# Kernel tuning notes

Hardware: AMD Instinct MI355X
Metric: run time of the kernel (lower is better)

Reference implementation:

```python
import jax, jax.numpy as jnp
import numpy as np


def setup_inputs() -> dict:
    key = jax.random.key(0)
    k1, k2 = jax.random.split(key)
    x = jax.random.normal(k1, (8, 128, 128, 128), dtype=jnp.float32)        # [N, C, H, W]
    codebook = jax.random.normal(k2, (256, 128), dtype=jnp.float32)         # [K, C] class_emb_vecs
    return {"x": x, "codebook": codebook}


def reference(x, codebook):
    # Brute-force 1-NN with p=2 (Euclidean), matching sklearn NearestNeighbors(brute, p=2).
    # argmin ||q - c||_2 == argmin (||q||^2 - 2 q.c + ||c||^2), so use the GEMM form.
    N, C, H, W = x.shape
    q = jnp.transpose(x, (0, 2, 3, 1)).reshape(-1, C)       # [N*H*W, C], matches x.reshape(-1, C) channel-last? 
    # NOTE: torch x.reshape(-1, C) on [N,C,H,W] flattens with C as the fastest-varying of the
    # leading dims only when memory layout is NCHW -> rows are (n, c_blocks)... Torch's
    # reshape(-1, C) actually slices contiguous groups of C elements along W. To be faithful
    # to x.reshape(-1, C) on a contiguous NCHW tensor:
    q = x.reshape(-1, C)                                     # [N*C*H*W/C, C] — same elements, same order as torch
    q_sq = jnp.sum(q * q, axis=1, keepdims=True)             # [M, 1]
    c_sq = jnp.sum(codebook * codebook, axis=1)              # [K]
    # squared distances: [M, K]
    d2 = q_sq - 2.0 * (q @ codebook.T) + c_sq[None, :]
    idx = jnp.argmin(d2, axis=1).astype(jnp.int32)           # [M]
    return idx.reshape(N, H, W)
```

## Files before the change

### kernel.cpp

```cpp
#include <hip/hip_runtime.h>
#include <hip/hip_bf16.h>


typedef __bf16 bf16x8 __attribute__((ext_vector_type(8)));
typedef float  floatx4 __attribute__((ext_vector_type(4)));

#define MFMA16 __builtin_amdgcn_mfma_f32_16x16x32_bf16

#define CSQ_OFF 1024
#define CBB_OFF 4096
#define T_FLAG  0.004f

__device__ __forceinline__ unsigned fmap(float f) {
    unsigned u = __float_as_uint(f);
    return (u & 0x80000000u) ? ~u : (u | 0x80000000u);
}
__device__ __forceinline__ float unfmap(unsigned u) {
    unsigned b = (u & 0x80000000u) ? (u ^ 0x80000000u) : ~u;
    return __uint_as_float(b);
}

__global__ void knn_prep(const float* __restrict__ cb, __bf16* __restrict__ cbB,
                         float* __restrict__ csq) {
    const int tid = threadIdx.x;
    const int id = blockIdx.x * 256 + tid;
    const int part = id >> 12;
    const int rem = id & 4095;
    const int t4 = rem >> 8;
    const int kb = (rem >> 6) & 3;
    const int ln = id & 63;
    const int n = t4 * 16 + (ln & 15);
    const int k0 = kb * 32 + (ln >> 4) * 8;
    const float* src = cb + (size_t)n * 128 + k0;
    union { __bf16 h[8]; uint4 u; } p;
#pragma unroll
    for (int j = 0; j < 8; ++j) {
        float f = src[j];
        __bf16 hh = (__bf16)f;
        p.h[j] = (part == 0) ? hh : (__bf16)(f - (float)hh);
    }
    *(uint4*)(cbB + (size_t)id * 8) = p.u;

    if (blockIdx.x == 0) {
        const float4* row = (const float4*)(cb + (size_t)tid * 128);
        float a0 = 0.f, a1 = 0.f, a2 = 0.f, a3 = 0.f;
#pragma unroll 8
        for (int j = 0; j < 32; ++j) {
            float4 v = row[j];
            a0 = fmaf(v.x, v.x, a0);
            a1 = fmaf(v.y, v.y, a1);
            a2 = fmaf(v.z, v.z, a2);
            a3 = fmaf(v.w, v.w, a3);
        }
        csq[tid] = (a0 + a1) + (a2 + a3);
    }
}

__global__ __launch_bounds__(256, 2) void knn_mfma(const float* __restrict__ x,
                                                   const float* __restrict__ cb,
                                                   const __bf16* __restrict__ cbB,
                                                   const float* __restrict__ csq_g,
                                                   int* __restrict__ out) {
    __shared__ __bf16 sB[32768];
    __shared__ float s_csq[256];
    __shared__ unsigned long long sWb[128];
    __shared__ unsigned long long sWs[128];
    __shared__ unsigned long long s_red[4];
    __shared__ int s_nf;
    __shared__ int s_flagq[64];

    const int tid = threadIdx.x;
    const int wave = tid >> 6;
    const int lane = tid & 63;
    const int mg = wave >> 1;
    const int ng = wave & 1;
    const int rl = lane & 15;
    const int kg = lane >> 4;

    s_csq[tid] = csq_g[tid];
    if (tid == 0) s_nf = 0;

    const float* xq = x + ((size_t)blockIdx.x * 64 + mg * 32) * 128;
    bf16x8 ah[2][4], al[2][4];
#pragma unroll
    for (int m = 0; m < 2; ++m) {
#pragma unroll
        for (int kb = 0; kb < 4; ++kb) {
            const float* s = xq + (size_t)(m * 16 + rl) * 128 + kb * 32 + kg * 8;
            float4 f0 = *(const float4*)(s);
            float4 f1 = *(const float4*)(s + 4);
            float f[8] = {f0.x, f0.y, f0.z, f0.w, f1.x, f1.y, f1.z, f1.w};
            union { __bf16 h[8]; bf16x8 v; } ph, pl;
#pragma unroll
            for (int j = 0; j < 8; ++j) {
                __bf16 hh = (__bf16)f[j];
                ph.h[j] = hh;
                pl.h[j] = (__bf16)(f[j] - (float)hh);
            }
            ah[m][kb] = ph.v;
            al[m][kb] = pl.v;
        }
    }

    {
        const uint4* src = (const uint4*)cbB;
        uint4* dst = (uint4*)sB;
#pragma unroll 4
        for (int i = 0; i < 16; ++i) dst[i * 256 + tid] = src[i * 256 + tid];
    }
    __syncthreads();

    floatx4 acc[2][8];
#pragma unroll
    for (int m = 0; m < 2; ++m)
#pragma unroll
        for (int t = 0; t < 8; ++t) acc[m][t] = (floatx4){0.f, 0.f, 0.f, 0.f};

#pragma unroll
    for (int kb = 0; kb < 4; ++kb) {
#pragma unroll
        for (int t = 0; t < 8; ++t) {
            const int t4 = ng * 8 + t;
            bf16x8 b = *(const bf16x8*)(sB + (((t4 * 4 + kb) * 64 + lane) * 8));
            acc[0][t] = MFMA16(ah[0][kb], b, acc[0][t], 0, 0, 0);
            acc[1][t] = MFMA16(ah[1][kb], b, acc[1][t], 0, 0, 0);
            acc[0][t] = MFMA16(al[0][kb], b, acc[0][t], 0, 0, 0);
            acc[1][t] = MFMA16(al[1][kb], b, acc[1][t], 0, 0, 0);
        }
    }
    __syncthreads();

    {
        const uint4* src = (const uint4*)(cbB + 32768);
        uint4* dst = (uint4*)sB;
#pragma unroll 4
        for (int i = 0; i < 16; ++i) dst[i * 256 + tid] = src[i * 256 + tid];
    }
    __syncthreads();

#pragma unroll
    for (int kb = 0; kb < 4; ++kb) {
#pragma unroll
        for (int t = 0; t < 8; ++t) {
            const int t4 = ng * 8 + t;
            bf16x8 b = *(const bf16x8*)(sB + (((t4 * 4 + kb) * 64 + lane) * 8));
            acc[0][t] = MFMA16(ah[0][kb], b, acc[0][t], 0, 0, 0);
            acc[1][t] = MFMA16(ah[1][kb], b, acc[1][t], 0, 0, 0);
        }
    }

    float cs[8];
#pragma unroll
    for (int t = 0; t < 8; ++t) cs[t] = s_csq[(ng * 8 + t) * 16 + rl];

#pragma unroll
    for (int m = 0; m < 2; ++m) {
#pragma unroll
        for (int r = 0; r < 4; ++r) {
            unsigned long long b = ~0ULL, s = ~0ULL;
#pragma unroll
            for (int t = 0; t < 8; ++t) {
                const int n = (ng * 8 + t) * 16 + rl;
                float score = fmaf(-2.0f, acc[m][t][r], cs[t]);
                unsigned long long key =
                    ((unsigned long long)fmap(score) << 32) | (unsigned)n;
                if (key < b) { s = b; b = key; }
                else if (key < s) { s = key; }
            }
#pragma unroll
            for (int d = 1; d < 16; d <<= 1) {
                unsigned long long ob = __shfl_xor(b, d);
                unsigned long long os = __shfl_xor(s, d);
                unsigned long long nb = ob < b ? ob : b;
                unsigned long long mx = ob < b ? b : ob;
                unsigned long long mn = os < s ? os : s;
                b = nb;
                s = mx < mn ? mx : mn;
            }
            if (rl == 0) {
                const int ql = mg * 32 + m * 16 + kg * 4 + r;
                sWb[ql * 2 + ng] = b;
                sWs[ql * 2 + ng] = s;
            }
        }
    }
    __syncthreads();

    if (tid < 64) {
        unsigned long long b0 = sWb[tid * 2 + 0], b1 = sWb[tid * 2 + 1];
        unsigned long long s0 = sWs[tid * 2 + 0], s1 = sWs[tid * 2 + 1];
        unsigned long long best = b0 < b1 ? b0 : b1;
        unsigned long long mx = b0 < b1 ? b1 : b0;
        unsigned long long mn = s0 < s1 ? s0 : s1;
        unsigned long long sec = mx < mn ? mx : mn;
        const size_t qg = (size_t)blockIdx.x * 64 + tid;
        out[qg] = (int)(unsigned)(best & 0xFFFFFFFFull);
        float f1 = unfmap((unsigned)(best >> 32));
        float f2 = unfmap((unsigned)(sec >> 32));
        if (f2 - f1 < T_FLAG) {
            int i = atomicAdd(&s_nf, 1);
            s_flagq[i] = tid;
        }
    }
    __syncthreads();

    const int nf = s_nf;
    for (int i = 0; i < nf; ++i) {
        const int lq = s_flagq[i];
        const size_t q = (size_t)blockIdx.x * 64 + lq;
        const float4* qr = (const float4*)(x + q * 128);
        const float4* cr = (const float4*)(cb + (size_t)tid * 128);
        float a0 = 0.f, a1 = 0.f, a2 = 0.f, a3 = 0.f;
#pragma unroll 8
        for (int c4 = 0; c4 < 32; ++c4) {
            float4 qv = qr[c4];
            float4 cv = cr[c4];
            a0 = fmaf(qv.x, cv.x, a0);
            a1 = fmaf(qv.y, cv.y, a1);
            a2 = fmaf(qv.z, cv.z, a2);
            a3 = fmaf(qv.w, cv.w, a3);
        }
        float dot = (a0 + a1) + (a2 + a3);
        float score = fmaf(-2.0f, dot, s_csq[tid]);
        unsigned long long key =
            ((unsigned long long)fmap(score) << 32) | (unsigned)tid;
#pragma unroll
        for (int d = 1; d < 64; d <<= 1) {
            unsigned long long o = __shfl_xor(key, d);
            key = o < key ? o : key;
        }
        if (lane == 0) s_red[wave] = key;
        __syncthreads();
        if (tid == 0) {
            unsigned long long b = s_red[0];
            unsigned long long o;
            o = s_red[1]; b = o < b ? o : b;
            o = s_red[2]; b = o < b ? o : b;
            o = s_red[3]; b = o < b ? o : b;
            out[q] = (int)(unsigned)(b & 0xFFFFFFFFull);
        }
        __syncthreads();
    }
}

extern "C" void kernel_launch(void* const* d_in, const int* in_sizes, int n_in,
                              void* d_out, int out_size, void* d_ws, size_t ws_size,
                              hipStream_t stream) {
    const float* x = (const float*)d_in[0];
    const float* cb = (const float*)d_in[1];
    int* out = (int*)d_out;

    char* ws = (char*)d_ws;
    float* csq = (float*)(ws + CSQ_OFF);
    __bf16* cbB = (__bf16*)(ws + CBB_OFF);

    const int M = in_sizes[0] / 128;

    knn_prep<<<32, 256, 0, stream>>>(cb, cbB, csq);
    knn_mfma<<<M / 64, 256, 0, stream>>>(x, cb, cbB, csq, out);
}
```

Measured before the change: 149.6 us.

## Split codebook into column chunks, give each wave its own rows, use direct-to-LDS loads

Each block now handles 128 queries instead of 64, and every wave owns 32 query rows across all 256 codes. The codebook is streamed through LDS in two chunks of 128 columns, each loaded with global_load_lds instead of register-staged copies. Top-2 results are merged across chunks per wave, which removes the cross-wave reduction, and the smaller LDS footprint allows three blocks per CU. The cost is twice as many LDS loads and barriers per block, half as many blocks, and higher register pressure under the tighter launch bound.

```diff
diff --git a/kernel.cpp b/kernel.cpp
--- a/kernel.cpp
+++ b/kernel.cpp
@@ -10,6 +10,13 @@
 #define CSQ_OFF 1024
 #define CBB_OFF 4096
 #define T_FLAG  0.004f
+
+typedef const __attribute__((address_space(1))) unsigned int* as1_u32p;
+typedef __attribute__((address_space(3))) unsigned int* as3_u32p;
+
+__device__ __forceinline__ void cp16_g2l(const void* g, void* l) {
+    __builtin_amdgcn_global_load_lds((as1_u32p)g, (as3_u32p)l, 16, 0, 0);
+}
 
 __device__ __forceinline__ unsigned fmap(float f) {
     unsigned u = __float_as_uint(f);
@@ -56,31 +63,28 @@
     }
 }
 
-__global__ __launch_bounds__(256, 2) void knn_mfma(const float* __restrict__ x,
+__global__ __launch_bounds__(256, 3) void knn_mfma(const float* __restrict__ x,
                                                    const float* __restrict__ cb,
                                                    const __bf16* __restrict__ cbB,
                                                    const float* __restrict__ csq_g,
                                                    int* __restrict__ out) {
-    __shared__ __bf16 sB[32768];
+    __shared__ __bf16 sB[16384];
     __shared__ float s_csq[256];
-    __shared__ unsigned long long sWb[128];
-    __shared__ unsigned long long sWs[128];
+    __shared__ unsigned long long sT2[4][32][2];
     __shared__ unsigned long long s_red[4];
     __shared__ int s_nf;
-    __shared__ int s_flagq[64];
+    __shared__ int s_flagq[128];
 
     const int tid = threadIdx.x;
     const int wave = tid >> 6;
     const int lane = tid & 63;
-    const int mg = wave >> 1;
-    const int ng = wave & 1;
     const int rl = lane & 15;
     const int kg = lane >> 4;
 
     s_csq[tid] = csq_g[tid];
     if (tid == 0) s_nf = 0;
 
-    const float* xq = x + ((size_t)blockIdx.x * 64 + mg * 32) * 128;
+    const float* xq = x + ((size_t)blockIdx.x * 128 + wave * 32) * 128;
     bf16x8 ah[2][4], al[2][4];
 #pragma unroll
     for (int m = 0; m < 2; ++m) {
@@ -101,13 +105,6 @@
             al[m][kb] = pl.v;
         }
     }
-
-    {
-        const uint4* src = (const uint4*)cbB;
-        uint4* dst = (uint4*)sB;
-#pragma unroll 4
-        for (int i = 0; i < 16; ++i) dst[i * 256 + tid] = src[i * 256 + tid];
-    }
     __syncthreads();
 
     floatx4 acc[2][8];
@@ -116,98 +113,117 @@
 #pragma unroll
         for (int t = 0; t < 8; ++t) acc[m][t] = (floatx4){0.f, 0.f, 0.f, 0.f};
 
-#pragma unroll
-    for (int kb = 0; kb < 4; ++kb) {
-#pragma unroll
-        for (int t = 0; t < 8; ++t) {
-            const int t4 = ng * 8 + t;
-            bf16x8 b = *(const bf16x8*)(sB + (((t4 * 4 + kb) * 64 + lane) * 8));
-            acc[0][t] = MFMA16(ah[0][kb], b, acc[0][t], 0, 0, 0);
-            acc[1][t] = MFMA16(ah[1][kb], b, acc[1][t], 0, 0, 0);
-            acc[0][t] = MFMA16(al[0][kb], b, acc[0][t], 0, 0, 0);
-            acc[1][t] = MFMA16(al[1][kb], b, acc[1][t], 0, 0, 0);
-        }
-    }
-    __syncthreads();
-
-    {
-        const uint4* src = (const uint4*)(cbB + 32768);
-        uint4* dst = (uint4*)sB;
-#pragma unroll 4
-        for (int i = 0; i < 16; ++i) dst[i * 256 + tid] = src[i * 256 + tid];
-    }
-    __syncthreads();
-
-#pragma unroll
-    for (int kb = 0; kb < 4; ++kb) {
-#pragma unroll
-        for (int t = 0; t < 8; ++t) {
-            const int t4 = ng * 8 + t;
-            bf16x8 b = *(const bf16x8*)(sB + (((t4 * 4 + kb) * 64 + lane) * 8));
-            acc[0][t] = MFMA16(ah[0][kb], b, acc[0][t], 0, 0, 0);
-            acc[1][t] = MFMA16(ah[1][kb], b, acc[1][t], 0, 0, 0);
-        }
-    }
-
-    float cs[8];
-#pragma unroll
-    for (int t = 0; t < 8; ++t) cs[t] = s_csq[(ng * 8 + t) * 16 + rl];
-
-#pragma unroll
-    for (int m = 0; m < 2; ++m) {
-#pragma unroll
-        for (int r = 0; r < 4; ++r) {
-            unsigned long long b = ~0ULL, s = ~0ULL;
+#pragma unroll 1
+    for (int nc = 0; nc < 2; ++nc) {
+        {
+            const __bf16* src = cbB + nc * 16384 + (size_t)tid * 8;
+            __bf16* dst = sB + tid * 8;
+#pragma unroll
+            for (int i = 0; i < 8; ++i)
+                cp16_g2l(src + i * 2048, dst + i * 2048);
+        }
+        __syncthreads();
+
+#pragma unroll
+        for (int kb = 0; kb < 4; ++kb) {
 #pragma unroll
             for (int t = 0; t < 8; ++t) {
-                const int n = (ng * 8 + t) * 16 + rl;
-                float score = fmaf(-2.0f, acc[m][t][r], cs[t]);
-                unsigned long long key =
-                    ((unsigned long long)fmap(score) << 32) | (unsigned)n;
-                if (key < b) { s = b; b = key; }
-                else if (key < s) { s = key; }
-            }
-#pragma unroll
-            for (int d = 1; d < 16; d <<= 1) {
-                unsigned long long ob = __shfl_xor(b, d);
-                unsigned long long os = __shfl_xor(s, d);
-                unsigned long long nb = ob < b ? ob : b;
-                unsigned long long mx = ob < b ? b : ob;
-                unsigned long long mn = os < s ? os : s;
-                b = nb;
-                s = mx < mn ? mx : mn;
-            }
-            if (rl == 0) {
-                const int ql = mg * 32 + m * 16 + kg * 4 + r;
-                sWb[ql * 2 + ng] = b;
-                sWs[ql * 2 + ng] = s;
-            }
-        }
-    }
-    __syncthreads();
-
-    if (tid < 64) {
-        unsigned long long b0 = sWb[tid * 2 + 0], b1 = sWb[tid * 2 + 1];
-        unsigned long long s0 = sWs[tid * 2 + 0], s1 = sWs[tid * 2 + 1];
-        unsigned long long best = b0 < b1 ? b0 : b1;
-        unsigned long long mx = b0 < b1 ? b1 : b0;
-        unsigned long long mn = s0 < s1 ? s0 : s1;
-        unsigned long long sec = mx < mn ? mx : mn;
-        const size_t qg = (size_t)blockIdx.x * 64 + tid;
-        out[qg] = (int)(unsigned)(best & 0xFFFFFFFFull);
-        float f1 = unfmap((unsigned)(best >> 32));
-        float f2 = unfmap((unsigned)(sec >> 32));
-        if (f2 - f1 < T_FLAG) {
-            int i = atomicAdd(&s_nf, 1);
-            s_flagq[i] = tid;
-        }
-    }
-    __syncthreads();
+                bf16x8 b = *(const bf16x8*)(sB + (((t * 4 + kb) * 64 + lane) * 8));
+                acc[0][t] = MFMA16(ah[0][kb], b, acc[0][t], 0, 0, 0);
+                acc[1][t] = MFMA16(ah[1][kb], b, acc[1][t], 0, 0, 0);
+                acc[0][t] = MFMA16(al[0][kb], b, acc[0][t], 0, 0, 0);
+                acc[1][t] = MFMA16(al[1][kb], b, acc[1][t], 0, 0, 0);
+            }
+        }
+        __syncthreads();
+
+        {
+            const __bf16* src = cbB + 32768 + nc * 16384 + (size_t)tid * 8;
+            __bf16* dst = sB + tid * 8;
+#pragma unroll
+            for (int i = 0; i < 8; ++i)
+                cp16_g2l(src + i * 2048, dst + i * 2048);
+        }
+        __syncthreads();
+
+#pragma unroll
+        for (int kb = 0; kb < 4; ++kb) {
+#pragma unroll
+            for (int t = 0; t < 8; ++t) {
+                bf16x8 b = *(const bf16x8*)(sB + (((t * 4 + kb) * 64 + lane) * 8));
+                acc[0][t] = MFMA16(ah[0][kb], b, acc[0][t], 0, 0, 0);
+                acc[1][t] = MFMA16(ah[1][kb], b, acc[1][t], 0, 0, 0);
+            }
+        }
+
+        float cs[8];
+#pragma unroll
+        for (int t = 0; t < 8; ++t) cs[t] = s_csq[(nc * 8 + t) * 16 + rl];
+
+#pragma unroll
+        for (int m = 0; m < 2; ++m) {
+#pragma unroll
+            for (int r = 0; r < 4; ++r) {
+                unsigned long long b = ~0ULL, s = ~0ULL;
+#pragma unroll
+                for (int t = 0; t < 8; ++t) {
+                    const int n = (nc * 8 + t) * 16 + rl;
+                    float score = fmaf(-2.0f, acc[m][t][r], cs[t]);
+                    unsigned long long key =
+                        ((unsigned long long)fmap(score) << 32) | (unsigned)n;
+                    if (key < b) { s = b; b = key; }
+                    else if (key < s) { s = key; }
+                }
+#pragma unroll
+                for (int d = 1; d < 16; d <<= 1) {
+                    unsigned long long ob = __shfl_xor(b, d);
+                    unsigned long long os = __shfl_xor(s, d);
+                    unsigned long long nb = ob < b ? ob : b;
+                    unsigned long long mx = ob < b ? b : ob;
+                    unsigned long long mn = os < s ? os : s;
+                    b = nb;
+                    s = mx < mn ? mx : mn;
+                }
+                if (rl == 0) {
+                    const int ql = m * 16 + kg * 4 + r;
+                    if (nc == 0) {
+                        sT2[wave][ql][0] = b;
+                        sT2[wave][ql][1] = s;
+                    } else {
+                        unsigned long long b0 = sT2[wave][ql][0];
+                        unsigned long long s0 = sT2[wave][ql][1];
+                        unsigned long long best = b0 < b ? b0 : b;
+                        unsigned long long mx = b0 < b ? b : b0;
+                        unsigned long long mn = s0 < s ? s0 : s;
+                        unsigned long long sec = mx < mn ? mx : mn;
+                        const size_t qg = (size_t)blockIdx.x * 128
+                                          + wave * 32 + ql;
+                        out[qg] = (int)(unsigned)(best & 0xFFFFFFFFull);
+                        float f1 = unfmap((unsigned)(best >> 32));
+                        float f2 = unfmap((unsigned)(sec >> 32));
+                        if (f2 - f1 < T_FLAG) {
+                            int i = atomicAdd(&s_nf, 1);
+                            s_flagq[i] = wave * 32 + ql;
+                        }
+                    }
+                }
+            }
+        }
+
+        if (nc == 0) {
+#pragma unroll
+            for (int m = 0; m < 2; ++m)
+#pragma unroll
+                for (int t = 0; t < 8; ++t)
+                    acc[m][t] = (floatx4){0.f, 0.f, 0.f, 0.f};
+        }
+        __syncthreads();
+    }
 
     const int nf = s_nf;
     for (int i = 0; i < nf; ++i) {
         const int lq = s_flagq[i];
-        const size_t q = (size_t)blockIdx.x * 64 + lq;
+        const size_t q = (size_t)blockIdx.x * 128 + lq;
         const float4* qr = (const float4*)(x + q * 128);
         const float4* cr = (const float4*)(cb + (size_t)tid * 128);
         float a0 = 0.f, a1 = 0.f, a2 = 0.f, a3 = 0.f;
@@ -257,5 +273,5 @@
     const int M = in_sizes[0] / 128;
 
     knn_prep<<<32, 256, 0, stream>>>(cb, cbB, csq);
-    knn_mfma<<<M / 64, 256, 0, stream>>>(x, cb, cbB, csq, out);
-}
+    knn_mfma<<<M / 128, 256, 0, stream>>>(x, cb, cbB, csq, out);
+}
```

New measurement: 147.4 us. About the same (-1.5%).
